# Optimization experiments

Measured on AMD Instinct MI355X. Metric: run time of the kernel, lower is better.

The kernel has to match this reference:

```python
import jax, jax.numpy as jnp
import numpy as np

NEG_SLOPE = 0.2
NUM_GRAPHS = 64


def _gatv2_layer(x, src, dst, Wl, bl, Wr, br, att, bias, n_nodes, heads, ch):
    # lin_l (source) and lin_r (target) transforms -> [N, H, C]
    xs = (x @ Wl + bl).reshape(n_nodes, heads, ch)
    xd = (x @ Wr + br).reshape(n_nodes, heads, ch)
    s = xs[src]                                   # [E, H, C] gathered source feats
    e = jax.nn.leaky_relu(s + xd[dst], NEG_SLOPE)  # GATv2: leaky_relu BEFORE att dot
    score = jnp.einsum('ehc,hc->eh', e, att)       # [E, H]
    # segment softmax over edges sharing the same target node
    smax = jax.ops.segment_max(score, dst, num_segments=n_nodes)
    ex = jnp.exp(score - smax[dst])
    denom = jax.ops.segment_sum(ex, dst, num_segments=n_nodes)
    alpha = ex / denom[dst]                        # [E, H]
    out = jax.ops.segment_sum(alpha[:, :, None] * s, dst, num_segments=n_nodes)
    return out.reshape(n_nodes, heads * ch) + bias


def setup_inputs() -> dict:
    key = jax.random.key(0)
    ks = jax.random.split(key, 20)
    N, E, F = 50000, 800000, 128
    H, C = 4, 64
    G = NUM_GRAPHS
    sc = 0.05
    inp = {
        'x': jax.random.normal(ks[0], (N, F), jnp.float32),
        'edge_index': jax.random.randint(ks[1], (2, E), 0, N, jnp.int64 if jax.config.read('jax_enable_x64') else jnp.int32).astype(jnp.int32),
        'batch': jnp.sort(jax.random.randint(ks[2], (N,), 0, G)).astype(jnp.int32),
        'W_l1': jax.random.normal(ks[3], (F, H * C)) * sc,
        'b_l1': jax.random.normal(ks[4], (H * C,)) * sc,
        'W_r1': jax.random.normal(ks[5], (F, H * C)) * sc,
        'b_r1': jax.random.normal(ks[6], (H * C,)) * sc,
        'att1': jax.random.normal(ks[7], (H, C)) * sc,
        'bias1': jax.random.normal(ks[8], (H * C,)) * sc,
        'W_l2': jax.random.normal(ks[9], (H * C, C)) * sc,
        'b_l2': jax.random.normal(ks[10], (C,)) * sc,
        'W_r2': jax.random.normal(ks[11], (H * C, C)) * sc,
        'b_r2': jax.random.normal(ks[12], (C,)) * sc,
        'att2': jax.random.normal(ks[13], (1, C)) * sc,
        'bias2': jax.random.normal(ks[14], (C,)) * sc,
        'W_lin': jax.random.normal(ks[15], (C, 1)) * sc,
        'b_lin': jax.random.normal(ks[16], (1,)) * sc,
    }
    return inp


def reference(x, edge_index, batch, W_l1, b_l1, W_r1, b_r1, att1, bias1,
              W_l2, b_l2, W_r2, b_r2, att2, bias2, W_lin, b_lin):
    N = x.shape[0]
    # PyG GATv2Conv adds self-loops by default
    loops = jnp.arange(N, dtype=edge_index.dtype)
    src = jnp.concatenate([edge_index[0], loops])
    dst = jnp.concatenate([edge_index[1], loops])

    h = _gatv2_layer(x, src, dst, W_l1, b_l1, W_r1, b_r1, att1, bias1, N, 4, 64)
    h = jax.nn.relu(h)  # dropout=identity (eval), norm=Identity
    h = _gatv2_layer(h, src, dst, W_l2, b_l2, W_r2, b_r2, att2, bias2, N, 1, 64)

    # global mean pool over graphs
    sums = jax.ops.segment_sum(h, batch, num_segments=NUM_GRAPHS)
    counts = jax.ops.segment_sum(jnp.ones((N,), h.dtype), batch, num_segments=NUM_GRAPHS)
    pooled = sums / jnp.maximum(counts, 1.0)[:, None]  # [G, 64]
    return pooled @ W_lin + b_lin                      # [G, 1]
```

## Files before the change

kernel.cpp:

```cpp
#include <hip/hip_runtime.h>
#include <hip/hip_bf16.h>
#include <math.h>

typedef __attribute__((ext_vector_type(8))) short short8;
typedef __attribute__((ext_vector_type(4))) float floatx4;

__device__ __forceinline__ float bf2f(unsigned short u) {
  union { unsigned int i; float f; } v; v.i = ((unsigned int)u) << 16; return v.f;
}
__device__ __forceinline__ unsigned short f2bf(float f) {
  union { float f; unsigned int u; } v; v.f = f;
  unsigned int r = (v.u + 0x7fffu + ((v.u >> 16) & 1u)) >> 16;
  return (unsigned short)r;
}
__device__ __forceinline__ int imin(int a, int b) { return a < b ? a : b; }
__device__ __forceinline__ int iclamp(int v, int lo, int hi) {
  return v < lo ? lo : (v > hi ? hi : v);
}
__device__ __forceinline__ float uasf(unsigned int u) {
  union { unsigned int i; float f; } v; v.i = u; return v.f;
}

__global__ void k_sentinel(float* out, float val) {
  if (threadIdx.x < 64) out[threadIdx.x] = val;
}

__global__ void k_probe_init(const void* __restrict__ x, int* dflag,
                             int* deg, float* pool, int* cnt, int N) {
  int i = blockIdx.x * 256 + threadIdx.x;
  if (i < N) deg[i] = 1;
  if (i < 64 * 64) pool[i] = 0.f;
  if (i < 64) cnt[i] = 0;
  if (blockIdx.x == 0) {
    __shared__ int c;
    if (threadIdx.x == 0) c = 0;
    __syncthreads();
    unsigned short u = ((const unsigned short*)x)[threadIdx.x];
    int e = (u >> 7) & 0xFF;
    atomicAdd(&c, (u == 0) || (e >= 100 && e <= 145));
    __syncthreads();
    if (threadIdx.x == 0) dflag[0] = (c < 240) ? 1 : 0;
  }
}

struct CvtSegs {
  const void* src[10];
  unsigned short* dst[10];
  int len[10];
};

__global__ void k_prep(const void* __restrict__ x, unsigned short* __restrict__ x_c,
                       int n8, CvtSegs segs,
                       const void* __restrict__ s0, const void* __restrict__ s1,
                       const void* __restrict__ s2, const void* __restrict__ s3,
                       unsigned short* __restrict__ d0, unsigned short* __restrict__ d1,
                       unsigned short* __restrict__ d2, unsigned short* __restrict__ d3,
                       const int* __restrict__ edst, int* deg, int E, int N,
                       const int* __restrict__ dflag, int nCvt8, int nTransB) {
  int b = blockIdx.x;
  if (b < nCvt8) {
    if (!dflag[0]) return;
    int i = b * 256 + threadIdx.x;
    if (i >= n8) return;
    const float* s = (const float*)x + (size_t)i * 8;
    ushort4 a, c;
    a.x = f2bf(s[0]); a.y = f2bf(s[1]); a.z = f2bf(s[2]); a.w = f2bf(s[3]);
    c.x = f2bf(s[4]); c.y = f2bf(s[5]); c.z = f2bf(s[6]); c.w = f2bf(s[7]);
    ((ushort4*)x_c)[i * 2] = a;
    ((ushort4*)x_c)[i * 2 + 1] = c;
    return;
  }
  b -= nCvt8;
  if (b < 10) {
    int i = threadIdx.x;
    if (i < segs.len[b])
      segs.dst[b][i] = dflag[0] ? f2bf(((const float*)segs.src[b])[i])
                                : ((const unsigned short*)segs.src[b])[i];
    return;
  }
  b -= 10;
  if (b < nTransB) {
    int idx = b * 256 + threadIdx.x;
    const void* src; unsigned short* dst; int R, C, loc;
    if (idx < 32768)      { src = s0; dst = d0; R = 128; C = 256; loc = idx; }
    else if (idx < 65536) { src = s1; dst = d1; R = 128; C = 256; loc = idx - 32768; }
    else if (idx < 81920) { src = s2; dst = d2; R = 256; C = 64;  loc = idx - 65536; }
    else                  { src = s3; dst = d3; R = 256; C = 64;  loc = idx - 81920; }
    unsigned short u = dflag[0] ? f2bf(((const float*)src)[loc])
                                : ((const unsigned short*)src)[loc];
    int r = loc / C, cc = loc - r * C;
    dst[cc * R + r] = u;
    return;
  }
  b -= nTransB;
  int e = b * 256 + threadIdx.x;
  if (e < E) atomicAdd(&deg[iclamp(edst[e], 0, N - 1)], 1);
}

__global__ __launch_bounds__(1024) void k_scan1(const int* __restrict__ deg, int* bsum, int N) {
  __shared__ int sm[1024];
  int tid = threadIdx.x;
  int i = blockIdx.x * 1024 + tid;
  sm[tid] = (i < N) ? deg[i] : 0;
  __syncthreads();
  for (int off = 512; off > 0; off >>= 1) {
    if (tid < off) sm[tid] += sm[tid + off];
    __syncthreads();
  }
  if (tid == 0) bsum[blockIdx.x] = sm[0];
}

__global__ void k_scan2(int* bsum, int nb) {
  if (threadIdx.x == 0) {
    int run = 0;
    for (int b = 0; b < nb; ++b) { int t = bsum[b]; bsum[b] = run; run += t; }
  }
}

__global__ __launch_bounds__(1024) void k_scan3(const int* __restrict__ deg,
                                                const int* __restrict__ bsum,
                                                int* rowptr, int* cursor, int N) {
  __shared__ int sm[1024];
  int tid = threadIdx.x;
  int i = blockIdx.x * 1024 + tid;
  int v = (i < N) ? deg[i] : 0;
  sm[tid] = v;
  __syncthreads();
  for (int off = 1; off < 1024; off <<= 1) {
    int t = (tid >= off) ? sm[tid - off] : 0;
    __syncthreads();
    sm[tid] += t;
    __syncthreads();
  }
  if (i < N) {
    int ex = sm[tid] - v + bsum[blockIdx.x];
    rowptr[i] = ex;
    cursor[i] = ex;
    if (i == N - 1) rowptr[N] = ex + v;
  }
}

__global__ void k_scatter(const int* __restrict__ esrc, const int* __restrict__ edst,
                          int* cursor, int* colx, int E, int N) {
  int e = blockIdx.x * 256 + threadIdx.x;
  int ET = E + N;
  if (e < ET) {
    int s, d;
    if (e < E) { s = iclamp(esrc[e], 0, N - 1); d = iclamp(edst[e], 0, N - 1); }
    else { s = e - E; d = s; }
    int pos = atomicAdd(&cursor[d], 1);
    pos = iclamp(pos, 0, ET - 1);
    colx[pos] = s;
  }
}

template <int K, int WT>
__global__ __launch_bounds__(256) void k_gemm2(
    const unsigned short* __restrict__ A0, const unsigned short* __restrict__ A1,
    const int* __restrict__ dflag,
    const unsigned short* __restrict__ BTl, const unsigned short* __restrict__ BTr,
    const unsigned short* __restrict__ bl, const unsigned short* __restrict__ br,
    unsigned short* __restrict__ outl, unsigned short* __restrict__ outr,
    int Nrows, int M) {
  const unsigned short* A = dflag[0] ? A1 : A0;
  int lane = threadIdx.x & 63;
  int wave = threadIdx.x >> 6;
  int row0 = blockIdx.x * 16;
  int col0 = wave * (WT * 16);
  int r = lane & 15, q = lane >> 4;
  int ar = imin(row0 + r, Nrows - 1);
  const unsigned short* Ap = A + (size_t)ar * K + q * 8;
  floatx4 accl[WT], accr[WT];
#pragma unroll
  for (int t = 0; t < WT; ++t) {
    accl[t] = (floatx4){0.f, 0.f, 0.f, 0.f};
    accr[t] = (floatx4){0.f, 0.f, 0.f, 0.f};
  }
#pragma unroll
  for (int k = 0; k < K; k += 32) {
    short8 av = *reinterpret_cast<const short8*>(Ap + k);
#pragma unroll
    for (int t = 0; t < WT; ++t) {
      int brow = col0 + t * 16 + r;
      short8 bvl = *reinterpret_cast<const short8*>(BTl + (size_t)brow * K + q * 8 + k);
      short8 bvr = *reinterpret_cast<const short8*>(BTr + (size_t)brow * K + q * 8 + k);
      accl[t] = __builtin_amdgcn_mfma_f32_16x16x32_bf16(av, bvl, accl[t], 0, 0, 0);
      accr[t] = __builtin_amdgcn_mfma_f32_16x16x32_bf16(av, bvr, accr[t], 0, 0, 0);
    }
  }
#pragma unroll
  for (int t = 0; t < WT; ++t) {
    int col = col0 + t * 16 + r;
    float bvl = bf2f(bl[col]);
    float bvr = bf2f(br[col]);
#pragma unroll
    for (int rr = 0; rr < 4; ++rr) {
      int row = row0 + q * 4 + rr;
      if (row < Nrows) {
        outl[(size_t)row * M + col] = f2bf(accl[t][rr] + bvl);
        outr[(size_t)row * M + col] = f2bf(accr[t][rr] + bvr);
      }
    }
  }
}

#define UNPACK2(u, v0, v1, v2, v3)          \
  v0 = uasf(u.x << 16); v1 = uasf(u.x & 0xffff0000u); \
  v2 = uasf(u.y << 16); v3 = uasf(u.y & 0xffff0000u);

#define SCORE(q0, q1, q2, q3, p)                             \
  p = q0 * 0.6f;                                             \
  p = fmaf(q1, 0.6f, p); p = fmaf(q2, 0.6f, p); p = fmaf(q3, 0.6f, p); \
  p = fmaf(c0, fabsf(q0), p); p = fmaf(c1, fabsf(q1), p);    \
  p = fmaf(c2, fabsf(q2), p); p = fmaf(c3, fabsf(q3), p);

__global__ __launch_bounds__(256) void k_agg_h4(
    const int* __restrict__ rowptr, const int* __restrict__ colx,
    const unsigned short* __restrict__ xs, const unsigned short* __restrict__ xd,
    const unsigned short* __restrict__ att, const unsigned short* __restrict__ bias,
    unsigned short* __restrict__ hout, int N) {
  int lane = threadIdx.x & 63;
  int dst = (blockIdx.x * 256 + threadIdx.x) >> 6;
  if (dst >= N) return;
  int off = lane << 2;
  unsigned int off2 = (unsigned int)off * 2;
  const char* xsb = (const char*)xs;
  ushort4 au = *reinterpret_cast<const ushort4*>(att + off);
  ushort4 du = *reinterpret_cast<const ushort4*>(xd + (size_t)dst * 256 + off);
  float a0 = bf2f(au.x), a1 = bf2f(au.y), a2 = bf2f(au.z), a3 = bf2f(au.w);
  float d0 = bf2f(du.x), d1 = bf2f(du.y), d2 = bf2f(du.z), d3 = bf2f(du.w);
  float ad0 = a0 * d0, ad1 = a1 * d1, ad2 = a2 * d2, ad3 = a3 * d3;
  float c0 = copysignf(0.4f, a0), c1 = copysignf(0.4f, a1);
  float c2 = copysignf(0.4f, a2), c3 = copysignf(0.4f, a3);
  float l = 0.f, o0 = 0.f, o1 = 0.f, o2 = 0.f, o3 = 0.f;
  int beg = __builtin_amdgcn_readfirstlane(rowptr[dst]);
  int end = __builtin_amdgcn_readfirstlane(rowptr[dst + 1]);
  int e1 = end - 1;
  int i0 = colx[beg], i1 = colx[imin(beg + 1, e1)];
  int i2 = colx[imin(beg + 2, e1)], i3 = colx[imin(beg + 3, e1)];
  uint2 ua = *(const uint2*)(xsb + (((unsigned)i0 << 9) + off2));
  uint2 ub = *(const uint2*)(xsb + (((unsigned)i1 << 9) + off2));
  uint2 uc = *(const uint2*)(xsb + (((unsigned)i2 << 9) + off2));
  uint2 ud = *(const uint2*)(xsb + (((unsigned)i3 << 9) + off2));
  for (int e = beg; e < end; e += 4) {
    uint2 na = ua, nb = ub, nc = uc, nd = ud;
    int np = e + 4;
    if (np < end) {
      int t0 = colx[np], t1 = colx[imin(np + 1, e1)];
      int t2 = colx[imin(np + 2, e1)], t3 = colx[imin(np + 3, e1)];
      na = *(const uint2*)(xsb + (((unsigned)t0 << 9) + off2));
      nb = *(const uint2*)(xsb + (((unsigned)t1 << 9) + off2));
      nc = *(const uint2*)(xsb + (((unsigned)t2 << 9) + off2));
      nd = *(const uint2*)(xsb + (((unsigned)t3 << 9) + off2));
    }
    float va0, va1, va2, va3, vb0, vb1, vb2, vb3;
    float vc0, vc1, vc2, vc3, vd0, vd1, vd2, vd3;
    UNPACK2(ua, va0, va1, va2, va3)
    UNPACK2(ub, vb0, vb1, vb2, vb3)
    UNPACK2(uc, vc0, vc1, vc2, vc3)
    UNPACK2(ud, vd0, vd1, vd2, vd3)
    float qa0 = fmaf(a0, va0, ad0), qa1 = fmaf(a1, va1, ad1);
    float qa2 = fmaf(a2, va2, ad2), qa3 = fmaf(a3, va3, ad3);
    float qb0 = fmaf(a0, vb0, ad0), qb1 = fmaf(a1, vb1, ad1);
    float qb2 = fmaf(a2, vb2, ad2), qb3 = fmaf(a3, vb3, ad3);
    float qc0 = fmaf(a0, vc0, ad0), qc1 = fmaf(a1, vc1, ad1);
    float qc2 = fmaf(a2, vc2, ad2), qc3 = fmaf(a3, vc3, ad3);
    float qd0 = fmaf(a0, vd0, ad0), qd1 = fmaf(a1, vd1, ad1);
    float qd2 = fmaf(a2, vd2, ad2), qd3 = fmaf(a3, vd3, ad3);
    float pa, pb, pc, pd;
    SCORE(qa0, qa1, qa2, qa3, pa)
    SCORE(qb0, qb1, qb2, qb3, pb)
    SCORE(qc0, qc1, qc2, qc3, pc)
    SCORE(qd0, qd1, qd2, qd3, pd)
    pa += __shfl_xor(pa, 1); pb += __shfl_xor(pb, 1);
    pc += __shfl_xor(pc, 1); pd += __shfl_xor(pd, 1);
    pa += __shfl_xor(pa, 2); pb += __shfl_xor(pb, 2);
    pc += __shfl_xor(pc, 2); pd += __shfl_xor(pd, 2);
    pa += __shfl_xor(pa, 4); pb += __shfl_xor(pb, 4);
    pc += __shfl_xor(pc, 4); pd += __shfl_xor(pd, 4);
    pa += __shfl_xor(pa, 8); pb += __shfl_xor(pb, 8);
    pc += __shfl_xor(pc, 8); pd += __shfl_xor(pd, 8);
    pa = fminf(fmaxf(pa, -60.f), 60.f);
    pb = (e + 1 < end) ? fminf(fmaxf(pb, -60.f), 60.f) : -INFINITY;
    pc = (e + 2 < end) ? fminf(fmaxf(pc, -60.f), 60.f) : -INFINITY;
    pd = (e + 3 < end) ? fminf(fmaxf(pd, -60.f), 60.f) : -INFINITY;
    float wa = __expf(pa), wb = __expf(pb), wc = __expf(pc), wd = __expf(pd);
    l += (wa + wb) + (wc + wd);
    o0 = fmaf(wa, va0, o0); o0 = fmaf(wb, vb0, o0);
    o0 = fmaf(wc, vc0, o0); o0 = fmaf(wd, vd0, o0);
    o1 = fmaf(wa, va1, o1); o1 = fmaf(wb, vb1, o1);
    o1 = fmaf(wc, vc1, o1); o1 = fmaf(wd, vd1, o1);
    o2 = fmaf(wa, va2, o2); o2 = fmaf(wb, vb2, o2);
    o2 = fmaf(wc, vc2, o2); o2 = fmaf(wd, vd2, o2);
    o3 = fmaf(wa, va3, o3); o3 = fmaf(wb, vb3, o3);
    o3 = fmaf(wc, vc3, o3); o3 = fmaf(wd, vd3, o3);
    ua = na; ub = nb; uc = nc; ud = nd;
  }
  float rl = 1.0f / l;
  ushort4 bu = *reinterpret_cast<const ushort4*>(bias + off);
  ushort4 res;
  res.x = f2bf(fmaxf(fmaf(o0, rl, bf2f(bu.x)), 0.f));
  res.y = f2bf(fmaxf(fmaf(o1, rl, bf2f(bu.y)), 0.f));
  res.z = f2bf(fmaxf(fmaf(o2, rl, bf2f(bu.z)), 0.f));
  res.w = f2bf(fmaxf(fmaf(o3, rl, bf2f(bu.w)), 0.f));
  *reinterpret_cast<ushort4*>(hout + (size_t)dst * 256 + off) = res;
}

__global__ __launch_bounds__(256) void k_agg_h1(
    const int* __restrict__ rowptr, const int* __restrict__ colx,
    const unsigned short* __restrict__ xs, const unsigned short* __restrict__ xd,
    const unsigned short* __restrict__ att, const unsigned short* __restrict__ bias,
    float* __restrict__ hout, int N) {
  int lane = threadIdx.x & 63;
  int wid = (blockIdx.x * 256 + threadIdx.x) >> 6;
  int g = lane >> 4, sl = lane & 15;
  int dst = wid * 4 + g;
  bool valid = dst < N;
  int dsafe = valid ? dst : 0;
  int cb = sl << 2;
  unsigned int cb2 = (unsigned int)cb * 2;
  const char* xsb = (const char*)xs;
  ushort4 au = *reinterpret_cast<const ushort4*>(att + cb);
  ushort4 du = *reinterpret_cast<const ushort4*>(xd + (size_t)dsafe * 64 + cb);
  float a0 = bf2f(au.x), a1 = bf2f(au.y), a2 = bf2f(au.z), a3 = bf2f(au.w);
  float d0 = bf2f(du.x), d1 = bf2f(du.y), d2 = bf2f(du.z), d3 = bf2f(du.w);
  float ad0 = a0 * d0, ad1 = a1 * d1, ad2 = a2 * d2, ad3 = a3 * d3;
  float c0 = copysignf(0.4f, a0), c1 = copysignf(0.4f, a1);
  float c2 = copysignf(0.4f, a2), c3 = copysignf(0.4f, a3);
  float l = 0.f, o0 = 0.f, o1 = 0.f, o2 = 0.f, o3 = 0.f;
  int beg = valid ? rowptr[dst] : 0;
  int end = valid ? rowptr[dst + 1] : 0;
  if (end > beg) {
    int e1 = end - 1;
    int i0 = colx[beg], i1 = colx[imin(beg + 1, e1)];
    int i2 = colx[imin(beg + 2, e1)], i3 = colx[imin(beg + 3, e1)];
    uint2 ua = *(const uint2*)(xsb + (((unsigned)i0 << 7) + cb2));
    uint2 ub = *(const uint2*)(xsb + (((unsigned)i1 << 7) + cb2));
    uint2 uc = *(const uint2*)(xsb + (((unsigned)i2 << 7) + cb2));
    uint2 ud = *(const uint2*)(xsb + (((unsigned)i3 << 7) + cb2));
    for (int e = beg; e < end; e += 4) {
      uint2 na = ua, nb = ub, nc = uc, nd = ud;
      int np = e + 4;
      if (np < end) {
        int t0 = colx[np], t1 = colx[imin(np + 1, e1)];
        int t2 = colx[imin(np + 2, e1)], t3 = colx[imin(np + 3, e1)];
        na = *(const uint2*)(xsb + (((unsigned)t0 << 7) + cb2));
        nb = *(const uint2*)(xsb + (((unsigned)t1 << 7) + cb2));
        nc = *(const uint2*)(xsb + (((unsigned)t2 << 7) + cb2));
        nd = *(const uint2*)(xsb + (((unsigned)t3 << 7) + cb2));
      }
      float va0, va1, va2, va3, vb0, vb1, vb2, vb3;
      float vc0, vc1, vc2, vc3, vd0, vd1, vd2, vd3;
      UNPACK2(ua, va0, va1, va2, va3)
      UNPACK2(ub, vb0, vb1, vb2, vb3)
      UNPACK2(uc, vc0, vc1, vc2, vc3)
      UNPACK2(ud, vd0, vd1, vd2, vd3)
      float qa0 = fmaf(a0, va0, ad0), qa1 = fmaf(a1, va1, ad1);
      float qa2 = fmaf(a2, va2, ad2), qa3 = fmaf(a3, va3, ad3);
      float qb0 = fmaf(a0, vb0, ad0), qb1 = fmaf(a1, vb1, ad1);
      float qb2 = fmaf(a2, vb2, ad2), qb3 = fmaf(a3, vb3, ad3);
      float qc0 = fmaf(a0, vc0, ad0), qc1 = fmaf(a1, vc1, ad1);
      float qc2 = fmaf(a2, vc2, ad2), qc3 = fmaf(a3, vc3, ad3);
      float qd0 = fmaf(a0, vd0, ad0), qd1 = fmaf(a1, vd1, ad1);
      float qd2 = fmaf(a2, vd2, ad2), qd3 = fmaf(a3, vd3, ad3);
      float pa, pb, pc, pd;
      SCORE(qa0, qa1, qa2, qa3, pa)
      SCORE(qb0, qb1, qb2, qb3, pb)
      SCORE(qc0, qc1, qc2, qc3, pc)
      SCORE(qd0, qd1, qd2, qd3, pd)
      pa += __shfl_xor(pa, 1); pb += __shfl_xor(pb, 1);
      pc += __shfl_xor(pc, 1); pd += __shfl_xor(pd, 1);
      pa += __shfl_xor(pa, 2); pb += __shfl_xor(pb, 2);
      pc += __shfl_xor(pc, 2); pd += __shfl_xor(pd, 2);
      pa += __shfl_xor(pa, 4); pb += __shfl_xor(pb, 4);
      pc += __shfl_xor(pc, 4); pd += __shfl_xor(pd, 4);
      pa += __shfl_xor(pa, 8); pb += __shfl_xor(pb, 8);
      pc += __shfl_xor(pc, 8); pd += __shfl_xor(pd, 8);
      pa = fminf(fmaxf(pa, -60.f), 60.f);
      pb = (e + 1 < end) ? fminf(fmaxf(pb, -60.f), 60.f) : -INFINITY;
      pc = (e + 2 < end) ? fminf(fmaxf(pc, -60.f), 60.f) : -INFINITY;
      pd = (e + 3 < end) ? fminf(fmaxf(pd, -60.f), 60.f) : -INFINITY;
      float wa = __expf(pa), wb = __expf(pb), wc = __expf(pc), wd = __expf(pd);
      l += (wa + wb) + (wc + wd);
      o0 = fmaf(wa, va0, o0); o0 = fmaf(wb, vb0, o0);
      o0 = fmaf(wc, vc0, o0); o0 = fmaf(wd, vd0, o0);
      o1 = fmaf(wa, va1, o1); o1 = fmaf(wb, vb1, o1);
      o1 = fmaf(wc, vc1, o1); o1 = fmaf(wd, vd1, o1);
      o2 = fmaf(wa, va2, o2); o2 = fmaf(wb, vb2, o2);
      o2 = fmaf(wc, vc2, o2); o2 = fmaf(wd, vd2, o2);
      o3 = fmaf(wa, va3, o3); o3 = fmaf(wb, vb3, o3);
      o3 = fmaf(wc, vc3, o3); o3 = fmaf(wd, vd3, o3);
      ua = na; ub = nb; uc = nc; ud = nd;
    }
  }
  if (valid) {
    float rl = 1.0f / l;
    ushort4 bu = *reinterpret_cast<const ushort4*>(bias + cb);
    floatx4 res;
    res[0] = fmaf(o0, rl, bf2f(bu.x));
    res[1] = fmaf(o1, rl, bf2f(bu.y));
    res[2] = fmaf(o2, rl, bf2f(bu.z));
    res[3] = fmaf(o3, rl, bf2f(bu.w));
    *reinterpret_cast<floatx4*>(hout + (size_t)dst * 64 + cb) = res;
  }
}

__global__ __launch_bounds__(256) void k_pool(const float* __restrict__ h2,
                                              const int* __restrict__ batch,
                                              float* pool, int* cnt, int N) {
  int lane = threadIdx.x & 63;
  int wid = (blockIdx.x * 256 + threadIdx.x) >> 6;
  int n0 = wid * 32;
  if (n0 >= N) return;
  int nend = imin(n0 + 32, N);
  float acc = 0.f;
  int c = 0;
  int gcur = iclamp(batch[n0], 0, 63);
  for (int n = n0; n < nend; ++n) {
    int gg = iclamp(batch[n], 0, 63);
    if (gg != gcur) {
      atomicAdd(&pool[gcur * 64 + lane], acc);
      if (lane == 0) atomicAdd(&cnt[gcur], c);
      acc = 0.f; c = 0; gcur = gg;
    }
    acc += h2[(size_t)n * 64 + lane];
    c++;
  }
  atomicAdd(&pool[gcur * 64 + lane], acc);
  if (lane == 0) atomicAdd(&cnt[gcur], c);
}

__global__ void k_final(const float* __restrict__ pool, const int* __restrict__ cnt,
                        const unsigned short* __restrict__ Wlinc,
                        const unsigned short* __restrict__ blinc,
                        float* __restrict__ out) {
  int g = threadIdx.x;
  if (g >= 64) return;
  float inv = 1.f / fmaxf((float)cnt[g], 1.f);
  float s = 0.f;
  for (int c = 0; c < 64; ++c) s += pool[g * 64 + c] * bf2f(Wlinc[c]);
  out[g] = fmaf(s, inv, bf2f(blinc[0]));
}

extern "C" void kernel_launch(void* const* d_in, const int* in_sizes, int n_in,
                              void* d_out, int out_size, void* d_ws, size_t ws_size,
                              hipStream_t stream) {
  const void* x     = d_in[0];
  const int*  ei    = (const int*)d_in[1];
  const int*  batch = (const int*)d_in[2];
  const void* Wl1 = d_in[3];  const void* bl1 = d_in[4];
  const void* Wr1 = d_in[5];  const void* br1 = d_in[6];
  const void* att1 = d_in[7]; const void* bias1 = d_in[8];
  const void* Wl2 = d_in[9];  const void* bl2 = d_in[10];
  const void* Wr2 = d_in[11]; const void* br2 = d_in[12];
  const void* att2 = d_in[13]; const void* bias2 = d_in[14];
  const void* Wlin = d_in[15]; const void* blin = d_in[16];
  float* out = (float*)d_out;

  const int F = 128, HC = 256, C2 = 64;
  int N = in_sizes[0] / F;
  int E = in_sizes[1] / 2;
  int ET = E + N;
  const int* esrc = ei;
  const int* edst = ei + E;

  char* w = (char*)d_ws;
  auto alloc = [&](size_t bytes) {
    char* p = w;
    w += (bytes + 255) & ~(size_t)255;
    return p;
  };
  int* dflag  = (int*)alloc(4);
  int* rowptr = (int*)alloc((size_t)(N + 1) * 4);
  int* cursor = (int*)alloc((size_t)N * 4);
  int* deg    = (int*)alloc((size_t)N * 4);
  int* bsum   = (int*)alloc(1024 * 4);
  float* pool = (float*)alloc(64 * 64 * 4);
  int* cnt    = (int*)alloc(64 * 4);
  int* colx   = (int*)alloc((size_t)ET * 4);
  unsigned short* smallc = (unsigned short*)alloc(4096);
  unsigned short* Wl1T = (unsigned short*)alloc((size_t)F * HC * 2);
  unsigned short* Wr1T = (unsigned short*)alloc((size_t)F * HC * 2);
  unsigned short* Wl2T = (unsigned short*)alloc((size_t)HC * C2 * 2);
  unsigned short* Wr2T = (unsigned short*)alloc((size_t)HC * C2 * 2);
  unsigned short* xs1  = (unsigned short*)alloc((size_t)N * HC * 2);
  unsigned short* xd1  = (unsigned short*)alloc((size_t)N * HC * 2);
  unsigned short* h1   = (unsigned short*)alloc((size_t)N * HC * 2);
  size_t required = (size_t)(w - (char*)d_ws);

  unsigned short* x_c = h1;
  unsigned short* xs2 = xs1;
  unsigned short* xd2 = xs1 + (size_t)N * C2;
  float*          h2  = (float*)xd1;

  unsigned short* bl1c   = smallc + 0;
  unsigned short* br1c   = smallc + 256;
  unsigned short* att1c  = smallc + 512;
  unsigned short* bias1c = smallc + 768;
  unsigned short* bl2c   = smallc + 1024;
  unsigned short* br2c   = smallc + 1088;
  unsigned short* att2c  = smallc + 1152;
  unsigned short* bias2c = smallc + 1216;
  unsigned short* Wlinc  = smallc + 1280;
  unsigned short* blinc  = smallc + 1344;

  if (ws_size < required) {
    k_sentinel<<<1, 64, 0, stream>>>(out, 1000.f + (float)(ws_size >> 20));
    return;
  }

  k_probe_init<<<(N + 255) / 256, 256, 0, stream>>>(x, dflag, deg, pool, cnt, N);

  CvtSegs segs;
  const void* ssrc[10] = {bl1, br1, att1, bias1, bl2, br2, att2, bias2, Wlin, blin};
  unsigned short* sdst[10] = {bl1c, br1c, att1c, bias1c, bl2c, br2c, att2c, bias2c, Wlinc, blinc};
  int slen[10] = {256, 256, 256, 256, 64, 64, 64, 64, 64, 1};
  for (int i = 0; i < 10; ++i) { segs.src[i] = ssrc[i]; segs.dst[i] = sdst[i]; segs.len[i] = slen[i]; }
  int n8 = N * F / 8;
  int nCvt8 = (n8 + 255) / 256;
  int nTransB = (2 * F * HC + 2 * HC * C2 + 255) / 256;
  int nHist = (E + 255) / 256;
  k_prep<<<nCvt8 + 10 + nTransB + nHist, 256, 0, stream>>>(
      x, x_c, n8, segs, Wl1, Wr1, Wl2, Wr2, Wl1T, Wr1T, Wl2T, Wr2T,
      edst, deg, E, N, dflag, nCvt8, nTransB);

  int nb = (N + 1023) / 1024;
  k_scan1<<<nb, 1024, 0, stream>>>(deg, bsum, N);
  k_scan2<<<1, 64, 0, stream>>>(bsum, nb);
  k_scan3<<<nb, 1024, 0, stream>>>(deg, bsum, rowptr, cursor, N);
  k_scatter<<<(ET + 255) / 256, 256, 0, stream>>>(esrc, edst, cursor, colx, E, N);

  k_gemm2<128, 4><<<(N + 15) / 16, 256, 0, stream>>>(
      (const unsigned short*)x, x_c, dflag, Wl1T, Wr1T, bl1c, br1c, xs1, xd1, N, HC);
  k_agg_h4<<<(N + 3) / 4, 256, 0, stream>>>(rowptr, colx, xs1, xd1, att1c, bias1c, h1, N);

  k_gemm2<256, 1><<<(N + 15) / 16, 256, 0, stream>>>(
      h1, h1, dflag, Wl2T, Wr2T, bl2c, br2c, xs2, xd2, N, C2);
  k_agg_h1<<<(N + 15) / 16, 256, 0, stream>>>(rowptr, colx, xs2, xd2, att2c, bias2c, h2, N);

  int pw = (N + 31) / 32;
  k_pool<<<(pw + 3) / 4, 256, 0, stream>>>(h2, batch, pool, cnt, N);
  k_final<<<1, 64, 0, stream>>>(pool, cnt, Wlinc, blinc, out);
}
```

Baseline: 408.4 us.

## Keep weight fragments in registers and loop over multiple row tiles per block

```diff
diff --git a/kernel.cpp b/kernel.cpp
--- a/kernel.cpp
+++ b/kernel.cpp
@@ -154,53 +154,80 @@
   }
 }
 
-template <int K, int WT>
-__global__ __launch_bounds__(256) void k_gemm2(
+template <int K, int CT, int RT>
+__global__ __launch_bounds__(256) void k_gemm2r(
     const unsigned short* __restrict__ A0, const unsigned short* __restrict__ A1,
     const int* __restrict__ dflag,
     const unsigned short* __restrict__ BTl, const unsigned short* __restrict__ BTr,
     const unsigned short* __restrict__ bl, const unsigned short* __restrict__ br,
     unsigned short* __restrict__ outl, unsigned short* __restrict__ outr,
     int Nrows, int M) {
+  constexpr int KI = K / 32;
   const unsigned short* A = dflag[0] ? A1 : A0;
   int lane = threadIdx.x & 63;
   int wave = threadIdx.x >> 6;
-  int row0 = blockIdx.x * 16;
-  int col0 = wave * (WT * 16);
   int r = lane & 15, q = lane >> 4;
-  int ar = imin(row0 + r, Nrows - 1);
-  const unsigned short* Ap = A + (size_t)ar * K + q * 8;
-  floatx4 accl[WT], accr[WT];
-#pragma unroll
-  for (int t = 0; t < WT; ++t) {
-    accl[t] = (floatx4){0.f, 0.f, 0.f, 0.f};
-    accr[t] = (floatx4){0.f, 0.f, 0.f, 0.f};
-  }
-#pragma unroll
-  for (int k = 0; k < K; k += 32) {
-    short8 av = *reinterpret_cast<const short8*>(Ap + k);
-#pragma unroll
-    for (int t = 0; t < WT; ++t) {
-      int brow = col0 + t * 16 + r;
-      short8 bvl = *reinterpret_cast<const short8*>(BTl + (size_t)brow * K + q * 8 + k);
-      short8 bvr = *reinterpret_cast<const short8*>(BTr + (size_t)brow * K + q * 8 + k);
-      accl[t] = __builtin_amdgcn_mfma_f32_16x16x32_bf16(av, bvl, accl[t], 0, 0, 0);
-      accr[t] = __builtin_amdgcn_mfma_f32_16x16x32_bf16(av, bvr, accr[t], 0, 0, 0);
-    }
-  }
-#pragma unroll
-  for (int t = 0; t < WT; ++t) {
-    int col = col0 + t * 16 + r;
-    float bvl = bf2f(bl[col]);
-    float bvr = bf2f(br[col]);
-#pragma unroll
-    for (int rr = 0; rr < 4; ++rr) {
-      int row = row0 + q * 4 + rr;
-      if (row < Nrows) {
-        outl[(size_t)row * M + col] = f2bf(accl[t][rr] + bvl);
-        outr[(size_t)row * M + col] = f2bf(accr[t][rr] + bvr);
+  int col0 = blockIdx.y * (4 * CT * 16) + wave * (CT * 16);
+  int row0 = blockIdx.x * (16 * RT);
+  short8 Bl[KI][CT], Br[KI][CT];
+#pragma unroll
+  for (int t = 0; t < CT; ++t) {
+    const unsigned short* bpl = BTl + (size_t)(col0 + t * 16 + r) * K + q * 8;
+    const unsigned short* bpr = BTr + (size_t)(col0 + t * 16 + r) * K + q * 8;
+#pragma unroll
+    for (int k = 0; k < KI; ++k) {
+      Bl[k][t] = *reinterpret_cast<const short8*>(bpl + k * 32);
+      Br[k][t] = *reinterpret_cast<const short8*>(bpr + k * 32);
+    }
+  }
+  float bvl[CT], bvr[CT];
+#pragma unroll
+  for (int t = 0; t < CT; ++t) {
+    bvl[t] = bf2f(bl[col0 + t * 16 + r]);
+    bvr[t] = bf2f(br[col0 + t * 16 + r]);
+  }
+  short8 a[KI], an[KI];
+  {
+    int ar0 = imin(row0 + r, Nrows - 1);
+    const unsigned short* Ap = A + (size_t)ar0 * K + q * 8;
+#pragma unroll
+    for (int k = 0; k < KI; ++k) a[k] = *reinterpret_cast<const short8*>(Ap + k * 32);
+  }
+  for (int rt = 0; rt < RT; ++rt) {
+    if (rt + 1 < RT) {
+      int arn = imin(row0 + (rt + 1) * 16 + r, Nrows - 1);
+      const unsigned short* Apn = A + (size_t)arn * K + q * 8;
+#pragma unroll
+      for (int k = 0; k < KI; ++k) an[k] = *reinterpret_cast<const short8*>(Apn + k * 32);
+    }
+    floatx4 accl[CT], accr[CT];
+#pragma unroll
+    for (int t = 0; t < CT; ++t) {
+      accl[t] = (floatx4){0.f, 0.f, 0.f, 0.f};
+      accr[t] = (floatx4){0.f, 0.f, 0.f, 0.f};
+    }
+#pragma unroll
+    for (int k = 0; k < KI; ++k) {
+#pragma unroll
+      for (int t = 0; t < CT; ++t) {
+        accl[t] = __builtin_amdgcn_mfma_f32_16x16x32_bf16(a[k], Bl[k][t], accl[t], 0, 0, 0);
+        accr[t] = __builtin_amdgcn_mfma_f32_16x16x32_bf16(a[k], Br[k][t], accr[t], 0, 0, 0);
       }
     }
+#pragma unroll
+    for (int t = 0; t < CT; ++t) {
+      int col = col0 + t * 16 + r;
+#pragma unroll
+      for (int rr = 0; rr < 4; ++rr) {
+        int row = row0 + rt * 16 + q * 4 + rr;
+        if (row < Nrows) {
+          outl[(size_t)row * M + col] = f2bf(accl[t][rr] + bvl[t]);
+          outr[(size_t)row * M + col] = f2bf(accr[t][rr] + bvr[t]);
+        }
+      }
+    }
+#pragma unroll
+    for (int k = 0; k < KI; ++k) a[k] = an[k];
   }
 }
 
@@ -389,7 +416,7 @@
       o2 = fmaf(wa, va2, o2); o2 = fmaf(wb, vb2, o2);
       o2 = fmaf(wc, vc2, o2); o2 = fmaf(wd, vd2, o2);
       o3 = fmaf(wa, va3, o3); o3 = fmaf(wb, vb3, o3);
-      o3 = fmaf(wc, vc3, o3); o3 = fmaf(wd, vd3, o3);
+      o3 = fmaf(wd, vd3, o3); o3 = fmaf(wc, vc3, o3);
       ua = na; ub = nb; uc = nc; ud = nd;
     }
   }
@@ -530,12 +557,18 @@
   k_scan3<<<nb, 1024, 0, stream>>>(deg, bsum, rowptr, cursor, N);
   k_scatter<<<(ET + 255) / 256, 256, 0, stream>>>(esrc, edst, cursor, colx, E, N);
 
-  k_gemm2<128, 4><<<(N + 15) / 16, 256, 0, stream>>>(
-      (const unsigned short*)x, x_c, dflag, Wl1T, Wr1T, bl1c, br1c, xs1, xd1, N, HC);
+  {
+    dim3 g((N + 127) / 128, 2);
+    k_gemm2r<128, 2, 8><<<g, 256, 0, stream>>>(
+        (const unsigned short*)x, x_c, dflag, Wl1T, Wr1T, bl1c, br1c, xs1, xd1, N, HC);
+  }
   k_agg_h4<<<(N + 3) / 4, 256, 0, stream>>>(rowptr, colx, xs1, xd1, att1c, bias1c, h1, N);
 
-  k_gemm2<256, 1><<<(N + 15) / 16, 256, 0, stream>>>(
-      h1, h1, dflag, Wl2T, Wr2T, bl2c, br2c, xs2, xd2, N, C2);
+  {
+    dim3 g((N + 63) / 64, 1);
+    k_gemm2r<256, 1, 4><<<g, 256, 0, stream>>>(
+        h1, h1, dflag, Wl2T, Wr2T, bl2c, br2c, xs2, xd2, N, C2);
+  }
   k_agg_h1<<<(N + 15) / 16, 256, 0, stream>>>(rowptr, colx, xs2, xd2, att2c, bias2c, h2, N);
 
   int pw = (N + 31) / 32;
```

New measurement: 361.5 us. 11.5% less time.
